# Performance work log

Measured on AMD Instinct MI355X. Metric: run time of the kernel, lower is better.

## Reference

```python
import jax, jax.numpy as jnp
import numpy as np

N_HEADS = 16
WINDOW = 128
EPS = 1e-6
NEG_INF = -1e30  # effectively -inf after softmax in fp32


def setup_inputs() -> dict:
    key = jax.random.key(0)
    ks = jax.random.split(key, 5)
    B, T, D = 2, 2048, 1024
    scale = 1.0 / np.sqrt(D)
    return {
        "x": jax.random.normal(ks[0], (B, T, D), dtype=jnp.float32),
        "Wq": jax.random.normal(ks[1], (D, D), dtype=jnp.float32) * scale,
        "Wk": jax.random.normal(ks[2], (D, D), dtype=jnp.float32) * scale,
        "Wv": jax.random.normal(ks[3], (D, D), dtype=jnp.float32) * scale,
        "Wo": jax.random.normal(ks[4], (D, D), dtype=jnp.float32) * scale,
    }


def _l2norm(t):
    # torch F.normalize: t / max(||t||, eps)
    n = jnp.sqrt(jnp.sum(t * t, axis=-1, keepdims=True))
    return t / jnp.maximum(n, EPS)


def reference(x, Wq, Wk, Wv, Wo):
    B, T, D = x.shape
    H, hd = N_HEADS, D // N_HEADS
    # projections (torch Linear: x @ W.T), split heads -> [B, H, T, hd]
    def proj(W):
        return jnp.einsum('btd,ed->bte', x, W).reshape(B, T, H, hd).transpose(0, 2, 1, 3)
    q = _l2norm(proj(Wq))
    k = _l2norm(proj(Wk))
    v = proj(Wv)
    # scores [B, H, T, T] (no 1/sqrt(d) scale in the source)
    attn = jnp.einsum('bhqd,bhkd->bhqk', q, k)
    pos = jnp.arange(T)
    rel = pos[None, :] - pos[:, None]            # rel[i, j] = j - i
    mask = (rel < 0) | (rel >= WINDOW)           # allowed: 0 <= j-i < window
    base = jnp.linspace(0.0, 1.0, H, dtype=x.dtype)
    slopes = jnp.power(jnp.asarray(2.0, x.dtype), -(8.0 * base))  # [H]
    alibi = -jnp.abs(rel).astype(x.dtype)[None, :, :] * slopes[:, None, None]  # [H,T,T]
    bias = jnp.where(mask[None, :, :], jnp.asarray(NEG_INF, x.dtype), alibi)
    attn = jax.nn.softmax(attn + bias[None], axis=-1)
    out = jnp.einsum('bhqk,bhkd->bhqd', attn, v)
    out = out.transpose(0, 2, 1, 3).reshape(B, T, D)
    return jnp.einsum('btd,ed->bte', out, Wo)
```

## Files before the change

kernel.cpp:

```cpp
#include <hip/hip_runtime.h>
#include <hip/hip_bf16.h>

#define T_SEQ   2048
#define BATCH   2
#define DMODEL  1024
#define NHEADS  16
#define HDIM    64
#define WINDOW  128

typedef __attribute__((ext_vector_type(8))) short bf16x8;
typedef __attribute__((ext_vector_type(4))) float f32x4;

#define LGKM(n)  asm volatile("s_waitcnt lgkmcnt(" #n ")" ::: "memory")
#define VMCNT(n) asm volatile("s_waitcnt vmcnt(" #n ")" ::: "memory")
#define SCHEDB() __builtin_amdgcn_sched_barrier(0)
#define BAR()    __builtin_amdgcn_s_barrier()

__device__ inline void gld_lds16(const __hip_bfloat16* g, __hip_bfloat16* l) {
    __builtin_amdgcn_global_load_lds(
        (const __attribute__((address_space(1))) unsigned int*)g,
        (__attribute__((address_space(3))) unsigned int*)l, 16, 0, 0);
}

__device__ inline bf16x8 ds_readb128(const __hip_bfloat16* p) {
    bf16x8 r;
    asm volatile("ds_read_b128 %0, %1"
                 : "=v"(r)
                 : "v"((const __attribute__((address_space(3))) __hip_bfloat16*)p));
    return r;
}

__global__ __launch_bounds__(256) void cvt_kernel(
    const float* __restrict__ x,  const float* __restrict__ Wq,
    const float* __restrict__ Wk, const float* __restrict__ Wv,
    const float* __restrict__ Wo,
    __hip_bfloat16* __restrict__ xb, __hip_bfloat16* __restrict__ Wb)
{
    const int lid = blockIdx.x;
    const float* src;
    __hip_bfloat16* dst;
    int blk;
    if (lid < 2048) { src = x; dst = xb; blk = lid; }
    else {
        int slot = (lid - 2048) >> 9;
        blk = (lid - 2048) & 511;
        src = (slot == 0) ? Wq : (slot == 1) ? Wk : (slot == 2) ? Wv : Wo;
        dst = Wb + (size_t)slot * 1024 * 1024;
    }
    int i = (blk * 256 + threadIdx.x) * 8;
    float4 a = *(const float4*)(src + i);
    float4 b = *(const float4*)(src + i + 4);
    __hip_bfloat16 pk[8] = {
        __float2bfloat16(a.x), __float2bfloat16(a.y),
        __float2bfloat16(a.z), __float2bfloat16(a.w),
        __float2bfloat16(b.x), __float2bfloat16(b.y),
        __float2bfloat16(b.z), __float2bfloat16(b.w)};
    *(uint4*)(dst + i) = *(uint4*)pk;
}

__global__ __launch_bounds__(512, 2) void gemm_qkv(
    const __hip_bfloat16* __restrict__ A,
    const __hip_bfloat16* __restrict__ Wp,
    __hip_bfloat16* __restrict__ C0,
    __hip_bfloat16* __restrict__ C1,
    __hip_bfloat16* __restrict__ C2)
{
    const int lid   = blockIdx.x;
    const int wgid  = (lid & 7) * 24 + (lid >> 3);
    const int bn    = wgid % 12;
    const int bm    = wgid / 12;
    const int m0    = bm * 256;
    const int n0    = bn * 256;
    const int z     = n0 >> 10;
    const int cbase = n0 & 1023;

    __shared__ __hip_bfloat16 S[4][2][256 * 32];

    const int t    = threadIdx.x;
    const int lane = t & 63;
    const int w    = t >> 6;
    const int wr   = w >> 2;
    const int wc   = w & 3;
    const int lrow = lane & 15;
    const int quad = lane >> 4;
    const int arow = wr * 128;
    const int brow = wc * 64;

    f32x4 acc[8][4];
#pragma unroll
    for (int i = 0; i < 8; ++i)
#pragma unroll
        for (int j = 0; j < 4; ++j)
            acc[i][j] = (f32x4){0.f, 0.f, 0.f, 0.f};

    auto STAGE = [&](int h) {
        const int slot = h & 3;
        const int k0   = h * 32;
        const int r    = (lane >> 2);
        const int c    = lane & 3;
#pragma unroll
        for (int i = 0; i < 2; ++i) {
            int row0 = i * 128 + w * 16;
            int row  = row0 + r;
            int gcx  = (c - row) & 3;
            gld_lds16(A + (size_t)(m0 + row) * DMODEL + k0 + gcx * 8,
                      &S[slot][0][row0 * 32]);
        }
#pragma unroll
        for (int i = 0; i < 2; ++i) {
            int row0 = i * 128 + w * 16;
            int row  = row0 + r;
            int gcx  = (c - row) & 3;
            gld_lds16(Wp + (size_t)(n0 + row) * DMODEL + k0 + gcx * 8,
                      &S[slot][1][row0 * 32]);
        }
    };

    auto RD = [&](const __hip_bfloat16* base, int r) -> bf16x8 {
        return ds_readb128(base + r * 32 + (((quad + r) & 3) << 3));
    };

    bf16x8 bf_[2][4], al_[2][4], ah_[2][4];

#define READS_BL(P, H) { \
    const __hip_bfloat16* Sb = &S[(H) & 3][1][0]; \
    const __hip_bfloat16* Sa = &S[(H) & 3][0][0]; \
    _Pragma("unroll") for (int ni = 0; ni < 4; ++ni) \
        bf_[P][ni] = RD(Sb, brow + ni * 16 + lrow); \
    _Pragma("unroll") for (int mi = 0; mi < 4; ++mi) \
        al_[P][mi] = RD(Sa, arow + mi * 16 + lrow); }

#define READS_AH(P, H) { \
    const __hip_bfloat16* Sa = &S[(H) & 3][0][0]; \
    _Pragma("unroll") for (int mi = 0; mi < 4; ++mi) \
        ah_[P][mi] = RD(Sa, arow + 64 + mi * 16 + lrow); }

#define MFMA_L(P) { \
    _Pragma("unroll") for (int mi = 0; mi < 4; ++mi) \
    _Pragma("unroll") for (int ni = 0; ni < 4; ++ni) \
        acc[mi][ni] = __builtin_amdgcn_mfma_f32_16x16x32_bf16( \
            al_[P][mi], bf_[P][ni], acc[mi][ni], 0, 0, 0); }

#define MFMA_H(P) { \
    _Pragma("unroll") for (int mi = 0; mi < 4; ++mi) \
    _Pragma("unroll") for (int ni = 0; ni < 4; ++ni) \
        acc[mi + 4][ni] = __builtin_amdgcn_mfma_f32_16x16x32_bf16( \
            ah_[P][mi], bf_[P][ni], acc[mi + 4][ni], 0, 0, 0); }

#define QBODY(H, P, PN, DO_STAGE, DO_READS, MIDGATE) { \
    if (DO_STAGE) STAGE((H) + 3); \
    LGKM(4); SCHEDB(); \
    __builtin_amdgcn_s_setprio(1); MFMA_L(P); __builtin_amdgcn_s_setprio(0); \
    if (DO_READS) READS_BL(PN, (H) + 1); \
    MIDGATE; SCHEDB(); \
    __builtin_amdgcn_s_setprio(1); MFMA_H(P); __builtin_amdgcn_s_setprio(0); \
    if (DO_READS) READS_AH(PN, (H) + 1); \
    VMCNT(4); BAR(); }

    STAGE(0); STAGE(1); STAGE(2);
    VMCNT(4);
    BAR();
    READS_BL(0, 0);
    READS_AH(0, 0);

    for (int it = 0; it < 15; ++it) {
        const int h = it * 2;
        QBODY(h,     0, 1, true,        true, LGKM(8));
        QBODY(h + 1, 1, 0, (it < 14),   true, LGKM(8));
    }
    QBODY(30, 0, 1, false, true,  LGKM(8));
    QBODY(31, 1, 0, false, false, LGKM(0));

#undef QBODY
#undef MFMA_H
#undef MFMA_L
#undef READS_AH
#undef READS_BL

    if (z != 2) {
#pragma unroll
        for (int mi = 0; mi < 8; ++mi) {
#pragma unroll
            for (int rr = 0; rr < 4; ++rr) {
                float ss = 0.f;
#pragma unroll
                for (int ni = 0; ni < 4; ++ni)
                    ss += acc[mi][ni][rr] * acc[mi][ni][rr];
                ss += __shfl_xor(ss, 1);
                ss += __shfl_xor(ss, 2);
                ss += __shfl_xor(ss, 4);
                ss += __shfl_xor(ss, 8);
                float inv = 1.0f / fmaxf(sqrtf(ss), 1e-6f);
#pragma unroll
                for (int ni = 0; ni < 4; ++ni)
                    acc[mi][ni][rr] *= inv;
            }
        }
    }

    __hip_bfloat16* C = (z == 0) ? C0 : (z == 1) ? C1 : C2;
#pragma unroll
    for (int mi = 0; mi < 8; ++mi) {
#pragma unroll
        for (int rr = 0; rr < 4; ++rr) {
            int row = m0 + arow + mi * 16 + quad * 4 + rr;
            __hip_bfloat16* Crow = C + (size_t)row * DMODEL + cbase + brow + lrow;
#pragma unroll
            for (int ni = 0; ni < 4; ++ni)
                Crow[ni * 16] = __float2bfloat16(acc[mi][ni][rr]);
        }
    }
}

__global__ __launch_bounds__(256, 2) void gemm_o(
    const __hip_bfloat16* __restrict__ A,
    const __hip_bfloat16* __restrict__ W,
    float* __restrict__ C)
{
    const int lid  = blockIdx.x;
    const int wgid = (lid & 7) * 32 + (lid >> 3);
    const int bn   = wgid & 7;
    const int bm   = wgid >> 3;
    const int m0   = bm * 128;
    const int n0   = bn * 128;

    __shared__ __hip_bfloat16 S[4][2][128 * 32];

    const int t    = threadIdx.x;
    const int lane = t & 63;
    const int wv   = t >> 6;
    const int lrow = lane & 15;
    const int quad = lane >> 4;
    const int wm   = (wv >> 1) * 64;
    const int wn   = (wv & 1) * 64;

    f32x4 acc[4][4];
#pragma unroll
    for (int i = 0; i < 4; ++i)
#pragma unroll
        for (int j = 0; j < 4; ++j)
            acc[i][j] = (f32x4){0.f, 0.f, 0.f, 0.f};

    auto STAGE = [&](int h) {
        const int slot = h & 3;
        const int k0   = h * 32;
        const int r    = (lane >> 2);
        const int c    = lane & 3;
#pragma unroll
        for (int i = 0; i < 2; ++i) {
            int row0 = i * 64 + wv * 16;
            int row  = row0 + r;
            int gcx  = (c - row) & 3;
            gld_lds16(A + (size_t)(m0 + row) * DMODEL + k0 + gcx * 8,
                      &S[slot][0][row0 * 32]);
        }
#pragma unroll
        for (int i = 0; i < 2; ++i) {
            int row0 = i * 64 + wv * 16;
            int row  = row0 + r;
            int gcx  = (c - row) & 3;
            gld_lds16(W + (size_t)(n0 + row) * DMODEL + k0 + gcx * 8,
                      &S[slot][1][row0 * 32]);
        }
    };

    auto RD = [&](const __hip_bfloat16* base, int r) -> bf16x8 {
        return ds_readb128(base + r * 32 + (((quad + r) & 3) << 3));
    };

    bf16x8 a_[2][4], b_[2][4];

#define READS_O(P, H) { \
    const __hip_bfloat16* Sa = &S[(H) & 3][0][0]; \
    const __hip_bfloat16* Sb = &S[(H) & 3][1][0]; \
    _Pragma("unroll") for (int mi = 0; mi < 4; ++mi) \
        a_[P][mi] = RD(Sa, wm + mi * 16 + lrow); \
    _Pragma("unroll") for (int ni = 0; ni < 4; ++ni) \
        b_[P][ni] = RD(Sb, wn + ni * 16 + lrow); }

#define OBODY(H, P, PN, DO_STAGE, DO_READS, GATE) { \
    if (DO_STAGE) STAGE((H) + 3); \
    if (DO_READS) READS_O(PN, (H) + 1); \
    GATE; SCHEDB(); \
    __builtin_amdgcn_s_setprio(1); \
    _Pragma("unroll") for (int mi = 0; mi < 4; ++mi) \
    _Pragma("unroll") for (int ni = 0; ni < 4; ++ni) \
        acc[mi][ni] = __builtin_amdgcn_mfma_f32_16x16x32_bf16( \
            a_[P][mi], b_[P][ni], acc[mi][ni], 0, 0, 0); \
    __builtin_amdgcn_s_setprio(0); \
    VMCNT(4); BAR(); }

    STAGE(0); STAGE(1); STAGE(2);
    VMCNT(4);
    BAR();
    READS_O(0, 0);

    for (int it = 0; it < 15; ++it) {
        const int h = it * 2;
        OBODY(h,     0, 1, true,      true, LGKM(8));
        OBODY(h + 1, 1, 0, (it < 14), true, LGKM(8));
    }
    OBODY(30, 0, 1, false, true,  LGKM(8));
    OBODY(31, 1, 0, false, false, LGKM(0));

#undef OBODY
#undef READS_O

#pragma unroll
    for (int mi = 0; mi < 4; ++mi) {
#pragma unroll
        for (int rr = 0; rr < 4; ++rr) {
            int row = m0 + wm + mi * 16 + quad * 4 + rr;
            float* Crow = C + (size_t)row * DMODEL + n0 + wn + lrow;
#pragma unroll
            for (int ni = 0; ni < 4; ++ni)
                Crow[ni * 16] = acc[mi][ni][rr];
        }
    }
}

__global__ __launch_bounds__(512) void attn_kernel(
    const __hip_bfloat16* __restrict__ Q,
    const __hip_bfloat16* __restrict__ K,
    const __hip_bfloat16* __restrict__ V,
    __hip_bfloat16* __restrict__ O)
{
    const int qb = blockIdx.x * 128;
    const int h  = blockIdx.y;
    const int b  = blockIdx.z;

    __shared__ __hip_bfloat16 KsP[8 * 16 * 168];
    __shared__ __hip_bfloat16 Vt[64 * 264];

    const size_t base = ((size_t)b * T_SEQ) * DMODEL + h * HDIM;
    const int t    = threadIdx.x;
    const int lane = t & 63;
    const int w    = t >> 6;

    {
        const int drow = lane >> 3, sl = lane & 7;
#pragma unroll
        for (int inst = 0; inst < 4; inst++) {
            int r0 = w * 32 + inst * 8;
            int r  = r0 + drow;
            int gcx = (sl - r) & 7;
            int j  = min(qb + r, T_SEQ - 1);
            gld_lds16(K + base + (size_t)j * DMODEL + gcx * 8, &KsP[r0 * 64]);
        }
    }
    if (t < 256) {
        int c  = t & 7;
        int b0 = t >> 3;
        int sg = (b0 & ~7) | ((b0 + c) & 7);
        unsigned short m[8][8];
#pragma unroll
        for (int i = 0; i < 8; i++) {
            int j = min(qb + b0 * 8 + i, T_SEQ - 1);
            uint4 u = *(const uint4*)(V + base + (size_t)j * DMODEL + c * 8);
            unsigned short tmp[8];
            *(uint4*)tmp = u;
#pragma unroll
            for (int e = 0; e < 8; e++) m[e][i] = tmp[e];
        }
#pragma unroll
        for (int e = 0; e < 8; e++)
            *(uint4*)&Vt[(c * 8 + e) * 264 + sg * 8] = *(uint4*)m[e];
    }
    if (t < 64) {
        uint4 zz = {0, 0, 0, 0};
        *(uint4*)&Vt[t * 264 + 256] = zz;
    }
    __syncthreads();

    const int col  = lane & 15;
    const int quad = lane >> 4;
    const float slope = exp2f(-8.0f * (float)h / 15.0f);

    const __hip_bfloat16* qp = Q + base + (size_t)(qb + w * 16 + col) * DMODEL + quad * 8;
    bf16x8 qf0 = *(const bf16x8*)(qp);
    bf16x8 qf1 = *(const bf16x8*)(qp + 32);

    f32x4 sc[9];
#pragma unroll
    for (int kt = 0; kt < 9; kt++) {
        sc[kt] = (f32x4){0.f, 0.f, 0.f, 0.f};
        int r = w * 16 + kt * 16 + col;
        bf16x8 kb0 = *(const bf16x8*)&KsP[r * 64 + ((quad     + r) & 7) * 8];
        bf16x8 kb1 = *(const bf16x8*)&KsP[r * 64 + ((quad + 4 + r) & 7) * 8];
        sc[kt] = __builtin_amdgcn_mfma_f32_16x16x32_bf16(qf0, kb0, sc[kt], 0, 0, 0);
        sc[kt] = __builtin_amdgcn_mfma_f32_16x16x32_bf16(qf1, kb1, sc[kt], 0, 0, 0);
    }

    float mx[4] = {-3e38f, -3e38f, -3e38f, -3e38f};
#pragma unroll
    for (int kt = 0; kt < 9; kt++) {
#pragma unroll
        for (int r = 0; r < 4; r++) {
            int ql  = quad * 4 + r;
            int rel = kt * 16 + col - ql;
            int ka  = qb + w * 16 + kt * 16 + col;
            bool valid = (rel >= 0) && (rel < WINDOW) && (ka < T_SEQ);
            float v = valid ? (sc[kt][r] - (float)rel * slope) : -1e30f;
            sc[kt][r] = v;
            mx[r] = fmaxf(mx[r], v);
        }
    }
#pragma unroll
    for (int r = 0; r < 4; r++) {
        mx[r] = fmaxf(mx[r], __shfl_xor(mx[r], 1));
        mx[r] = fmaxf(mx[r], __shfl_xor(mx[r], 2));
        mx[r] = fmaxf(mx[r], __shfl_xor(mx[r], 4));
        mx[r] = fmaxf(mx[r], __shfl_xor(mx[r], 8));
    }
    float sm[4] = {0.f, 0.f, 0.f, 0.f};
#pragma unroll
    for (int kt = 0; kt < 9; kt++) {
#pragma unroll
        for (int r = 0; r < 4; r++) {
            float e = __expf(sc[kt][r] - mx[r]);
            sc[kt][r] = e;
            sm[r] += e;
        }
    }
#pragma unroll
    for (int r = 0; r < 4; r++) {
        sm[r] += __shfl_xor(sm[r], 1);
        sm[r] += __shfl_xor(sm[r], 2);
        sm[r] += __shfl_xor(sm[r], 4);
        sm[r] += __shfl_xor(sm[r], 8);
        sm[r] = 1.0f / sm[r];
    }

    __syncthreads();
    __hip_bfloat16* Ps = KsP + w * (16 * 168);
#pragma unroll
    for (int kt = 0; kt < 9; kt++)
#pragma unroll
        for (int r = 0; r < 4; r++)
            Ps[(quad * 4 + r) * 168 + kt * 16 + col] = __float2bfloat16(sc[kt][r] * sm[r]);
#pragma unroll
    for (int i = 0; i < 4; i++)
        Ps[(lane & 15) * 168 + 144 + quad * 4 + i] = __float2bfloat16(0.f);
    __syncthreads();

    f32x4 o[4];
#pragma unroll
    for (int nd = 0; nd < 4; nd++) o[nd] = (f32x4){0.f, 0.f, 0.f, 0.f};
#pragma unroll
    for (int kc = 0; kc < 5; kc++) {
        bf16x8 pf = *(const bf16x8*)&Ps[col * 168 + kc * 32 + quad * 8];
        int bblk = w * 2 + kc * 4 + quad;
#pragma unroll
        for (int nd = 0; nd < 4; nd++) {
            int d  = nd * 16 + col;
            int sg = (bblk < 32) ? ((bblk & ~7) | ((bblk + (d >> 3)) & 7)) : 32;
            bf16x8 vf = *(const bf16x8*)&Vt[d * 264 + sg * 8];
            o[nd] = __builtin_amdgcn_mfma_f32_16x16x32_bf16(pf, vf, o[nd], 0, 0, 0);
        }
    }

#pragma unroll
    for (int r = 0; r < 4; r++) {
        __hip_bfloat16* op = O + base + (size_t)(qb + w * 16 + quad * 4 + r) * DMODEL + col;
#pragma unroll
        for (int nd = 0; nd < 4; nd++)
            op[nd * 16] = __float2bfloat16(o[nd][r]);
    }
}

extern "C" void kernel_launch(void* const* d_in, const int* in_sizes, int n_in,
                              void* d_out, int out_size, void* d_ws, size_t ws_size,
                              hipStream_t stream)
{
    const float* x  = (const float*)d_in[0];
    const float* Wq = (const float*)d_in[1];
    const float* Wk = (const float*)d_in[2];
    const float* Wv = (const float*)d_in[3];
    const float* Wo = (const float*)d_in[4];
    float* out = (float*)d_out;

    const size_t MT = (size_t)BATCH * T_SEQ;
    __hip_bfloat16* Qw = (__hip_bfloat16*)d_ws;
    __hip_bfloat16* Kw = Qw + MT * DMODEL;
    __hip_bfloat16* Vw = Kw + MT * DMODEL;
    __hip_bfloat16* XA = Vw + MT * DMODEL;
    __hip_bfloat16* Wb = XA + MT * DMODEL;

    cvt_kernel<<<4096, 256, 0, stream>>>(x, Wq, Wk, Wv, Wo, XA, Wb);

    gemm_qkv<<<dim3(192), 512, 0, stream>>>(XA, Wb, Qw, Kw, Vw);

    dim3 g2(T_SEQ / 128, NHEADS, BATCH);
    attn_kernel<<<g2, 512, 0, stream>>>(Qw, Kw, Vw, XA);

    gemm_o<<<dim3(256), 256, 0, stream>>>(XA, Wb + 3 * 1024 * 1024, out);
}
```

Before: 148.5 us.

## Retile QKV GEMM to 128x128 blocks with 64-wide K double buffering

Rewrites the fused QKV projection GEMM to use 128x128 output tiles with 256 threads and 768 workgroups instead of 256x256 tiles with 512 threads and 192 workgroups. It stages K in chunks of 64 into a two-deep LDS buffer with an 8-way XOR swizzle, splitting each chunk into two MFMA halves. The output projection GEMM's LDS swizzle changes to use row>>1, aiming to reduce bank conflicts for its 32-wide rows. The intent is to fill more CUs and reduce tail imbalance. The cost is less data reuse per tile and a shallower prefetch pipeline.

```diff
diff --git a/kernel.cpp b/kernel.cpp
--- a/kernel.cpp
+++ b/kernel.cpp
@@ -58,7 +58,7 @@
     *(uint4*)(dst + i) = *(uint4*)pk;
 }
 
-__global__ __launch_bounds__(512, 2) void gemm_qkv(
+__global__ __launch_bounds__(256, 2) void gemm_qkv(
     const __hip_bfloat16* __restrict__ A,
     const __hip_bfloat16* __restrict__ Wp,
     __hip_bfloat16* __restrict__ C0,
@@ -66,120 +66,111 @@
     __hip_bfloat16* __restrict__ C2)
 {
     const int lid   = blockIdx.x;
-    const int wgid  = (lid & 7) * 24 + (lid >> 3);
-    const int bn    = wgid % 12;
-    const int bm    = wgid / 12;
-    const int m0    = bm * 256;
-    const int n0    = bn * 256;
+    const int wgid  = (lid & 7) * 96 + (lid >> 3);
+    const int bn    = wgid % 24;
+    const int bm    = wgid / 24;
+    const int m0    = bm * 128;
+    const int n0    = bn * 128;
     const int z     = n0 >> 10;
     const int cbase = n0 & 1023;
 
-    __shared__ __hip_bfloat16 S[4][2][256 * 32];
+    __shared__ __hip_bfloat16 S[2][2][128 * 64];
 
     const int t    = threadIdx.x;
     const int lane = t & 63;
-    const int w    = t >> 6;
-    const int wr   = w >> 2;
-    const int wc   = w & 3;
+    const int wv   = t >> 6;
     const int lrow = lane & 15;
     const int quad = lane >> 4;
-    const int arow = wr * 128;
-    const int brow = wc * 64;
-
-    f32x4 acc[8][4];
-#pragma unroll
-    for (int i = 0; i < 8; ++i)
+    const int wm   = (wv >> 1) * 64;
+    const int wn   = (wv & 1) * 64;
+    const int drow = lane >> 3;
+    const int sl   = lane & 7;
+
+    f32x4 acc[4][4];
+#pragma unroll
+    for (int i = 0; i < 4; ++i)
 #pragma unroll
         for (int j = 0; j < 4; ++j)
             acc[i][j] = (f32x4){0.f, 0.f, 0.f, 0.f};
 
-    auto STAGE = [&](int h) {
-        const int slot = h & 3;
-        const int k0   = h * 32;
-        const int r    = (lane >> 2);
-        const int c    = lane & 3;
-#pragma unroll
-        for (int i = 0; i < 2; ++i) {
-            int row0 = i * 128 + w * 16;
-            int row  = row0 + r;
-            int gcx  = (c - row) & 3;
-            gld_lds16(A + (size_t)(m0 + row) * DMODEL + k0 + gcx * 8,
-                      &S[slot][0][row0 * 32]);
-        }
-#pragma unroll
-        for (int i = 0; i < 2; ++i) {
-            int row0 = i * 128 + w * 16;
-            int row  = row0 + r;
-            int gcx  = (c - row) & 3;
-            gld_lds16(Wp + (size_t)(n0 + row) * DMODEL + k0 + gcx * 8,
-                      &S[slot][1][row0 * 32]);
+    auto STAGE = [&](int tile, int buf) {
+        const int k0 = tile << 6;
+#pragma unroll
+        for (int inst = 0; inst < 4; ++inst) {
+            int r0 = wv * 32 + inst * 8;
+            int r  = r0 + drow;
+            int gcx = (sl - r) & 7;
+            gld_lds16(A + (size_t)(m0 + r) * DMODEL + k0 + gcx * 8,
+                      &S[buf][0][r0 * 64]);
+        }
+#pragma unroll
+        for (int inst = 0; inst < 4; ++inst) {
+            int r0 = wv * 32 + inst * 8;
+            int r  = r0 + drow;
+            int gcx = (sl - r) & 7;
+            gld_lds16(Wp + (size_t)(n0 + r) * DMODEL + k0 + gcx * 8,
+                      &S[buf][1][r0 * 64]);
         }
     };
 
-    auto RD = [&](const __hip_bfloat16* base, int r) -> bf16x8 {
-        return ds_readb128(base + r * 32 + (((quad + r) & 3) << 3));
+    auto RDA = [&](int buf, int mi, int kc) -> bf16x8 {
+        int r = wm + mi * 16 + lrow;
+        return ds_readb128(&S[buf][0][r * 64 + (((kc + r) & 7) << 3)]);
     };
-
-    bf16x8 bf_[2][4], al_[2][4], ah_[2][4];
-
-#define READS_BL(P, H) { \
-    const __hip_bfloat16* Sb = &S[(H) & 3][1][0]; \
-    const __hip_bfloat16* Sa = &S[(H) & 3][0][0]; \
-    _Pragma("unroll") for (int ni = 0; ni < 4; ++ni) \
-        bf_[P][ni] = RD(Sb, brow + ni * 16 + lrow); \
-    _Pragma("unroll") for (int mi = 0; mi < 4; ++mi) \
-        al_[P][mi] = RD(Sa, arow + mi * 16 + lrow); }
-
-#define READS_AH(P, H) { \
-    const __hip_bfloat16* Sa = &S[(H) & 3][0][0]; \
-    _Pragma("unroll") for (int mi = 0; mi < 4; ++mi) \
-        ah_[P][mi] = RD(Sa, arow + 64 + mi * 16 + lrow); }
-
-#define MFMA_L(P) { \
-    _Pragma("unroll") for (int mi = 0; mi < 4; ++mi) \
-    _Pragma("unroll") for (int ni = 0; ni < 4; ++ni) \
-        acc[mi][ni] = __builtin_amdgcn_mfma_f32_16x16x32_bf16( \
-            al_[P][mi], bf_[P][ni], acc[mi][ni], 0, 0, 0); }
-
-#define MFMA_H(P) { \
-    _Pragma("unroll") for (int mi = 0; mi < 4; ++mi) \
-    _Pragma("unroll") for (int ni = 0; ni < 4; ++ni) \
-        acc[mi + 4][ni] = __builtin_amdgcn_mfma_f32_16x16x32_bf16( \
-            ah_[P][mi], bf_[P][ni], acc[mi + 4][ni], 0, 0, 0); }
-
-#define QBODY(H, P, PN, DO_STAGE, DO_READS, MIDGATE) { \
-    if (DO_STAGE) STAGE((H) + 3); \
-    LGKM(4); SCHEDB(); \
-    __builtin_amdgcn_s_setprio(1); MFMA_L(P); __builtin_amdgcn_s_setprio(0); \
-    if (DO_READS) READS_BL(PN, (H) + 1); \
-    MIDGATE; SCHEDB(); \
-    __builtin_amdgcn_s_setprio(1); MFMA_H(P); __builtin_amdgcn_s_setprio(0); \
-    if (DO_READS) READS_AH(PN, (H) + 1); \
-    VMCNT(4); BAR(); }
-
-    STAGE(0); STAGE(1); STAGE(2);
-    VMCNT(4);
+    auto RDB = [&](int buf, int ni, int kc) -> bf16x8 {
+        int r = wn + ni * 16 + lrow;
+        return ds_readb128(&S[buf][1][r * 64 + (((kc + r) & 7) << 3)]);
+    };
+
+    bf16x8 a0[4], b0[4], a1[4], b1[4];
+
+    STAGE(0, 0);
+    VMCNT(0);
     BAR();
-    READS_BL(0, 0);
-    READS_AH(0, 0);
-
-    for (int it = 0; it < 15; ++it) {
-        const int h = it * 2;
-        QBODY(h,     0, 1, true,        true, LGKM(8));
-        QBODY(h + 1, 1, 0, (it < 14),   true, LGKM(8));
-    }
-    QBODY(30, 0, 1, false, true,  LGKM(8));
-    QBODY(31, 1, 0, false, false, LGKM(0));
-
-#undef QBODY
-#undef MFMA_H
-#undef MFMA_L
-#undef READS_AH
-#undef READS_BL
+#pragma unroll
+    for (int mi = 0; mi < 4; ++mi) a0[mi] = RDA(0, mi, quad);
+#pragma unroll
+    for (int ni = 0; ni < 4; ++ni) b0[ni] = RDB(0, ni, quad);
+
+#pragma unroll 2
+    for (int tt = 0; tt < 16; ++tt) {
+        const int cur = tt & 1, nxt = cur ^ 1;
+        if (tt < 15) STAGE(tt + 1, nxt);
+#pragma unroll
+        for (int mi = 0; mi < 4; ++mi) a1[mi] = RDA(cur, mi, 4 + quad);
+#pragma unroll
+        for (int ni = 0; ni < 4; ++ni) b1[ni] = RDB(cur, ni, 4 + quad);
+        LGKM(8); SCHEDB();
+        __builtin_amdgcn_s_setprio(1);
+#pragma unroll
+        for (int mi = 0; mi < 4; ++mi)
+#pragma unroll
+            for (int ni = 0; ni < 4; ++ni)
+                acc[mi][ni] = __builtin_amdgcn_mfma_f32_16x16x32_bf16(
+                    a0[mi], b0[ni], acc[mi][ni], 0, 0, 0);
+        __builtin_amdgcn_s_setprio(0);
+        VMCNT(0);
+        LGKM(0); SCHEDB();
+        BAR();
+        if (tt < 15) {
+#pragma unroll
+            for (int mi = 0; mi < 4; ++mi) a0[mi] = RDA(nxt, mi, quad);
+#pragma unroll
+            for (int ni = 0; ni < 4; ++ni) b0[ni] = RDB(nxt, ni, quad);
+        }
+        __builtin_amdgcn_s_setprio(1);
+#pragma unroll
+        for (int mi = 0; mi < 4; ++mi)
+#pragma unroll
+            for (int ni = 0; ni < 4; ++ni)
+                acc[mi][ni] = __builtin_amdgcn_mfma_f32_16x16x32_bf16(
+                    a1[mi], b1[ni], acc[mi][ni], 0, 0, 0);
+        __builtin_amdgcn_s_setprio(0);
+    }
 
     if (z != 2) {
 #pragma unroll
-        for (int mi = 0; mi < 8; ++mi) {
+        for (int mi = 0; mi < 4; ++mi) {
 #pragma unroll
             for (int rr = 0; rr < 4; ++rr) {
                 float ss = 0.f;
@@ -200,11 +191,11 @@
 
     __hip_bfloat16* C = (z == 0) ? C0 : (z == 1) ? C1 : C2;
 #pragma unroll
-    for (int mi = 0; mi < 8; ++mi) {
+    for (int mi = 0; mi < 4; ++mi) {
 #pragma unroll
         for (int rr = 0; rr < 4; ++rr) {
-            int row = m0 + arow + mi * 16 + quad * 4 + rr;
-            __hip_bfloat16* Crow = C + (size_t)row * DMODEL + cbase + brow + lrow;
+            int row = m0 + wm + mi * 16 + quad * 4 + rr;
+            __hip_bfloat16* Crow = C + (size_t)row * DMODEL + cbase + wn + lrow;
 #pragma unroll
             for (int ni = 0; ni < 4; ++ni)
                 Crow[ni * 16] = __float2bfloat16(acc[mi][ni][rr]);
@@ -250,7 +241,7 @@
         for (int i = 0; i < 2; ++i) {
             int row0 = i * 64 + wv * 16;
             int row  = row0 + r;
-            int gcx  = (c - row) & 3;
+            int gcx  = (c - (row >> 1)) & 3;
             gld_lds16(A + (size_t)(m0 + row) * DMODEL + k0 + gcx * 8,
                       &S[slot][0][row0 * 32]);
         }
@@ -258,14 +249,14 @@
         for (int i = 0; i < 2; ++i) {
             int row0 = i * 64 + wv * 16;
             int row  = row0 + r;
-            int gcx  = (c - row) & 3;
+            int gcx  = (c - (row >> 1)) & 3;
             gld_lds16(W + (size_t)(n0 + row) * DMODEL + k0 + gcx * 8,
                       &S[slot][1][row0 * 32]);
         }
     };
 
     auto RD = [&](const __hip_bfloat16* base, int r) -> bf16x8 {
-        return ds_readb128(base + r * 32 + (((quad + r) & 3) << 3));
+        return ds_readb128(base + r * 32 + (((quad + (r >> 1)) & 3) << 3));
     };
 
     bf16x8 a_[2][4], b_[2][4];
@@ -488,7 +479,7 @@
 
     cvt_kernel<<<4096, 256, 0, stream>>>(x, Wq, Wk, Wv, Wo, XA, Wb);
 
-    gemm_qkv<<<dim3(192), 512, 0, stream>>>(XA, Wb, Qw, Kw, Vw);
+    gemm_qkv<<<dim3(768), 256, 0, stream>>>(XA, Wb, Qw, Kw, Vw);
 
     dim3 g2(T_SEQ / 128, NHEADS, BATCH);
     attn_kernel<<<g2, 512, 0, stream>>>(Qw, Kw, Vw, XA);
```

Result: slower. 151.8 us (+2.2%).
